# Performance work log

Measured on AMD Instinct MI355X. Metric: run time of the kernel, lower is better.

The kernel has to match this reference:

```python
import jax, jax.numpy as jnp
import numpy as np

N, IN, H, D, OUT = 2048, 256, 12, 32, 384
ALPHA = 0.2


def setup_inputs() -> dict:
    key = jax.random.key(0)
    ks = jax.random.split(key, 12)
    s = 0.05
    return {
        "x": jax.random.normal(ks[0], (N, IN), jnp.float32),
        "adj": jax.random.uniform(ks[1], (N, N), jnp.float32),  # all > 0 -> fully connected mask
        "W": jax.random.normal(ks[2], (H * D, IN), jnp.float32) * s,
        "attn_src": jax.random.normal(ks[3], (H, D), jnp.float32) * s,
        "attn_dst": jax.random.normal(ks[4], (H, D), jnp.float32) * s,
        "edge_W": jax.random.normal(ks[5], (H, 1), jnp.float32) * s,
        "edge_b": jax.random.normal(ks[6], (H,), jnp.float32) * s,
        "res_W": jax.random.normal(ks[7], (H * D, IN), jnp.float32) * s,
        "res_b": jax.random.normal(ks[8], (H * D,), jnp.float32) * s,
        "fus_W": jax.random.normal(ks[9], (OUT, H * D), jnp.float32) * s,
        "fus_b": jax.random.normal(ks[10], (OUT,), jnp.float32) * s,
    }


def reference(x, adj, W, attn_src, attn_dst, edge_W, edge_b, res_W, res_b, fus_W, fus_b):
    n = x.shape[0]
    h = (x @ W.T).reshape(n, H, D)                      # [N,H,D]
    a_src = jnp.einsum("nhd,hd->nh", h, attn_src)       # [N,H]
    a_dst = jnp.einsum("nhd,hd->nh", h, attn_dst)       # [N,H]
    attn = a_src[:, None, :] + a_dst[None, :, :]        # [N,N,H]
    # edge_encoder: Linear(1 -> H) applied to adj[...,None]
    attn = attn + adj[..., None] * edge_W.reshape(1, 1, H) + edge_b
    mask = (adj > 0)[..., None]                         # [N,N,1]
    attn = jnp.where(mask, attn, -jnp.inf)
    attn = jnp.where(attn >= 0, attn, ALPHA * attn)     # leaky_relu
    attn = jax.nn.softmax(attn, axis=1)                 # over source nodes j
    # dropout is identity in eval mode
    h_out = jnp.einsum("ijh,jhd->ihd", attn, h).reshape(n, H * D)
    h_out = h_out + x @ res_W.T + res_b                 # residual
    out = jax.nn.gelu(h_out @ fus_W.T + fus_b, approximate=False)
    return out
```

## Files before the change

### kernel.cpp

```cpp
#include <hip/hip_runtime.h>
#include <hip/hip_bf16.h>

#define NN 2048
#define NH 12
#define HD 32
#define CALL 384

typedef float f32x16 __attribute__((ext_vector_type(16)));
typedef _Float16 f16x4 __attribute__((ext_vector_type(4)));

static __device__ __forceinline__ f32x16 mfma8f16(f16x4 a, f16x4 b, f32x16 c) {
    return __builtin_amdgcn_mfma_f32_32x32x8f16(a, b, c, 0, 0, 0);
}
static __device__ __forceinline__ f16x4 u2f(uint2 u) {
    union { uint2 u2; f16x4 f; } c; c.u2 = u; return c.f;
}

__global__ __launch_bounds__(512) void gemm01(
    const float* __restrict__ A, const float* __restrict__ B0,
    const float* __restrict__ B1, const float* __restrict__ bias1,
    const float* __restrict__ attn_src, const float* __restrict__ attn_dst,
    _Float16* __restrict__ outT, float* __restrict__ outF,
    float* __restrict__ asrc, float* __restrict__ adstT)
{
    __shared__ __align__(16) char smem[17408];
    _Float16 (*As)[68] = (_Float16(*)[68])(smem);
    _Float16 (*Bs)[68] = (_Float16(*)[68])(smem + 8704);
    float* red = (float*)smem;

    const int t = threadIdx.x;
    const int w = t >> 6, l = t & 63, g = l >> 5, il = l & 31;
    const int q = w & 3, kg = w >> 2;
    const int m0 = blockIdx.x * 64, n0 = blockIdx.y * 64;
    const int mode = blockIdx.z;
    const float* B = mode ? B1 : B0;
    const int wr = (q >> 1) * 32, wc = (q & 1) * 32;
    const int ti = t >> 3, seg = t & 7;
    const int Kdim = 256;

    f32x16 acc;
#pragma unroll
    for (int r = 0; r < 16; ++r) acc[r] = 0.f;

#pragma unroll 1
    for (int ss = 0; ss < 4; ++ss) {
        const int kk = ss * 64;
        __syncthreads();
        {
            const float* Ap = A + (size_t)(m0 + ti) * Kdim + kk + seg * 8;
            float4 v0 = *reinterpret_cast<const float4*>(Ap);
            float4 v1 = *reinterpret_cast<const float4*>(Ap + 4);
            f16x4 lo = {(_Float16)v0.x, (_Float16)v0.y, (_Float16)v0.z, (_Float16)v0.w};
            f16x4 hi = {(_Float16)v1.x, (_Float16)v1.y, (_Float16)v1.z, (_Float16)v1.w};
            *reinterpret_cast<f16x4*>(&As[ti][seg * 8])     = lo;
            *reinterpret_cast<f16x4*>(&As[ti][seg * 8 + 4]) = hi;
        }
        {
            const float* Bp = B + (size_t)(n0 + ti) * Kdim + kk + seg * 8;
            float4 v0 = *reinterpret_cast<const float4*>(Bp);
            float4 v1 = *reinterpret_cast<const float4*>(Bp + 4);
            f16x4 lo = {(_Float16)v0.x, (_Float16)v0.y, (_Float16)v0.z, (_Float16)v0.w};
            f16x4 hi = {(_Float16)v1.x, (_Float16)v1.y, (_Float16)v1.z, (_Float16)v1.w};
            *reinterpret_cast<f16x4*>(&Bs[ti][seg * 8])     = lo;
            *reinterpret_cast<f16x4*>(&Bs[ti][seg * 8 + 4]) = hi;
        }
        __syncthreads();
#pragma unroll
        for (int kc = 0; kc < 4; ++kc) {
            f16x4 af = *reinterpret_cast<const f16x4*>(&As[wr + il][kg * 32 + kc * 8 + 4 * g]);
            f16x4 bf = *reinterpret_cast<const f16x4*>(&Bs[wc + il][kg * 32 + kc * 8 + 4 * g]);
            acc = mfma8f16(af, bf, acc);
        }
    }

    __syncthreads();
    if (kg == 1) {
#pragma unroll
        for (int r = 0; r < 16; ++r) red[(q * 16 + r) * 64 + l] = acc[r];
    }
    __syncthreads();
    if (kg != 0) return;
#pragma unroll
    for (int r = 0; r < 16; ++r) acc[r] += red[(q * 16 + r) * 64 + l];

    const int colg = n0 + wc + il;
    if (mode == 0) {
#pragma unroll
        for (int p = 0; p < 4; ++p) {
            const int row = m0 + wr + 8 * p + 4 * g;
            f16x4 v;
#pragma unroll
            for (int r = 0; r < 4; ++r) v[r] = (_Float16)acc[4 * p + r];
            *reinterpret_cast<f16x4*>(&outT[(size_t)colg * NN + row]) = v;
        }
        const int hstar = colg >> 5;
        const float sv = attn_src[hstar * HD + il];
        const float dv = attn_dst[hstar * HD + il];
        float ps[16], pd[16];
#pragma unroll
        for (int r = 0; r < 16; ++r) { ps[r] = acc[r] * sv; pd[r] = acc[r] * dv; }
#pragma unroll
        for (int m = 1; m <= 16; m <<= 1) {
#pragma unroll
            for (int r = 0; r < 16; ++r) {
                ps[r] += __shfl_xor(ps[r], m);
                pd[r] += __shfl_xor(pd[r], m);
            }
        }
        if (il == 0) {
#pragma unroll
            for (int r = 0; r < 16; ++r) {
                const int row = m0 + wr + (r & 3) + 8 * (r >> 2) + 4 * g;
                asrc[row * NH + hstar] = ps[r];
                adstT[(size_t)hstar * NN + row] = pd[r] * 1.44269504089f;
            }
        }
    } else {
        const float bs = bias1[colg];
#pragma unroll
        for (int r = 0; r < 16; ++r) {
            const int row = m0 + wr + (r & 3) + 8 * (r >> 2) + 4 * g;
            outF[(size_t)row * CALL + colg] = acc[r] + bs;
        }
    }
}

__global__ __launch_bounds__(512) void gemm2(
    const _Float16* __restrict__ A16, const float* __restrict__ B,
    const float* __restrict__ bias, float* __restrict__ outF)
{
    __shared__ __align__(16) char smem[17408];
    _Float16 (*As)[68] = (_Float16(*)[68])(smem);
    _Float16 (*Bs)[68] = (_Float16(*)[68])(smem + 8704);
    float* red = (float*)smem;

    const int t = threadIdx.x;
    const int w = t >> 6, l = t & 63, g = l >> 5, il = l & 31;
    const int q = w & 3, kg = w >> 2;
    const int m0 = blockIdx.x * 64, n0 = blockIdx.y * 64;
    const int wr = (q >> 1) * 32, wc = (q & 1) * 32;
    const int ti = t >> 3, seg = t & 7;
    const int Kdim = 384;

    f32x16 acc;
#pragma unroll
    for (int r = 0; r < 16; ++r) acc[r] = 0.f;

#pragma unroll 1
    for (int ss = 0; ss < 6; ++ss) {
        const int kk = ss * 64;
        __syncthreads();
        {
            const uint4 v = *reinterpret_cast<const uint4*>(A16 + (size_t)(m0 + ti) * Kdim + kk + seg * 8);
            *reinterpret_cast<uint2*>(&As[ti][seg * 8])     = make_uint2(v.x, v.y);
            *reinterpret_cast<uint2*>(&As[ti][seg * 8 + 4]) = make_uint2(v.z, v.w);
        }
        {
            const float* Bp = B + (size_t)(n0 + ti) * Kdim + kk + seg * 8;
            float4 v0 = *reinterpret_cast<const float4*>(Bp);
            float4 v1 = *reinterpret_cast<const float4*>(Bp + 4);
            f16x4 lo = {(_Float16)v0.x, (_Float16)v0.y, (_Float16)v0.z, (_Float16)v0.w};
            f16x4 hi = {(_Float16)v1.x, (_Float16)v1.y, (_Float16)v1.z, (_Float16)v1.w};
            *reinterpret_cast<f16x4*>(&Bs[ti][seg * 8])     = lo;
            *reinterpret_cast<f16x4*>(&Bs[ti][seg * 8 + 4]) = hi;
        }
        __syncthreads();
#pragma unroll
        for (int kc = 0; kc < 4; ++kc) {
            f16x4 af = *reinterpret_cast<const f16x4*>(&As[wr + il][kg * 32 + kc * 8 + 4 * g]);
            f16x4 bf = *reinterpret_cast<const f16x4*>(&Bs[wc + il][kg * 32 + kc * 8 + 4 * g]);
            acc = mfma8f16(af, bf, acc);
        }
    }

    __syncthreads();
    if (kg == 1) {
#pragma unroll
        for (int r = 0; r < 16; ++r) red[(q * 16 + r) * 64 + l] = acc[r];
    }
    __syncthreads();
    if (kg != 0) return;
#pragma unroll
    for (int r = 0; r < 16; ++r) acc[r] += red[(q * 16 + r) * 64 + l];

    const int colg = n0 + wc + il;
    const float bs = bias[colg];
#pragma unroll
    for (int r = 0; r < 16; ++r) {
        const int row = m0 + wr + (r & 3) + 8 * (r >> 2) + 4 * g;
        float vv = acc[r] + bs;
        vv = 0.5f * vv * (1.0f + erff(vv * 0.70710678118f));
        outF[(size_t)row * CALL + colg] = vv;
    }
}

__global__ __launch_bounds__(1024, 4) void attn6(
    const float* __restrict__ adj, const _Float16* __restrict__ hT,
    const float* __restrict__ asrc, const float* __restrict__ adstT,
    const float* __restrict__ eW, const float* __restrict__ eb,
    const float* __restrict__ res, _Float16* __restrict__ hsum)
{
    __shared__ __align__(16) char smem[55296];
    const int t = threadIdx.x;
    const int w = t >> 6, l = t & 63, g = l >> 5, il = l & 31;
    const int band = blockIdx.x & 63, hg = blockIdx.x >> 6;
    const int i0 = band * 32, h0 = hg * 3, c0 = hg * 96;

    float* adst_s = (float*)(smem + w * 1536);
    float* red    = (float*)smem;
    float* dsum_s = (float*)(smem + 49152);

    const float LOG2E = 1.44269504089f;
    float base_h[3], eWr[3];
#pragma unroll
    for (int hh = 0; hh < 3; ++hh) {
        base_h[hh] = (asrc[(size_t)(i0 + il) * NH + h0 + hh] + eb[h0 + hh]) * LOG2E;
        eWr[hh] = eW[h0 + hh] * LOG2E;
    }

    const int jbase = w * 128;
#pragma unroll
    for (int p = 0; p < 6; ++p) {
        const int idx = p * 64 + l;
        adst_s[idx] = adstT[(size_t)(h0 + (idx >> 7)) * NN + jbase + (idx & 127)];
    }

    f32x16 acc[3];
#pragma unroll
    for (int hh = 0; hh < 3; ++hh)
#pragma unroll
        for (int r = 0; r < 16; ++r) acc[hh][r] = 0.f;
    float dsum[3] = {0.f, 0.f, 0.f};

    const _Float16* hbase = hT  + (size_t)(c0 + il) * NN + jbase + 16 * g;
    const float*    abase = adj + (size_t)(i0 + il) * NN + jbase + 16 * g;

    float4 ajc[4], ajn[4];
#pragma unroll
    for (int p = 0; p < 4; ++p)
        ajc[p] = *reinterpret_cast<const float4*>(abase + 4 * p);

#pragma unroll 1
    for (int tl = 0; tl < 4; ++tl) {
        const int jo = tl * 32;
        if (tl < 3) {
#pragma unroll
            for (int p = 0; p < 4; ++p)
                ajn[p] = *reinterpret_cast<const float4*>(abase + jo + 32 + 4 * p);
        }
#pragma unroll
        for (int hh = 0; hh < 3; ++hh) {
            const _Float16* hp = hbase + (size_t)(hh * 32) * NN + jo;
            const uint4 hA = *reinterpret_cast<const uint4*>(hp);
            const uint4 hB = *reinterpret_cast<const uint4*>(hp + 8);
#pragma unroll
            for (int ks = 0; ks < 4; ++ks) {
                const float4 a4 = ajc[ks];
                const float4 ad = *reinterpret_cast<const float4*>(
                    &adst_s[hh * 128 + jo + 16 * g + 4 * ks]);
                f16x4 ef;
#pragma unroll
                for (int jj = 0; jj < 4; ++jj) {
                    const float ajv = (&a4.x)[jj];
                    float tt = fmaf(ajv, eWr[hh], base_h[hh] + (&ad.x)[jj]);
                    tt = fmaxf(tt, 0.2f * tt);
                    const float ee = ajv > 0.f ? exp2f(tt) : 0.f;
                    dsum[hh] += ee;
                    ef[jj] = (_Float16)ee;
                }
                const uint2 hu = (ks == 0) ? make_uint2(hA.x, hA.y)
                               : (ks == 1) ? make_uint2(hA.z, hA.w)
                               : (ks == 2) ? make_uint2(hB.x, hB.y)
                                           : make_uint2(hB.z, hB.w);
                acc[hh] = mfma8f16(ef, u2f(hu), acc[hh]);
            }
        }
#pragma unroll
        for (int p = 0; p < 4; ++p) ajc[p] = ajn[p];
    }

    __syncthreads();
#pragma unroll
    for (int hh = 0; hh < 3; ++hh) {
        const float dtot = dsum[hh] + __shfl_xor(dsum[hh], 32);
        if (g == 0) dsum_s[(w * 3 + hh) * 32 + il] = dtot;
    }
    if (w < 4) {
#pragma unroll
        for (int hh = 0; hh < 3; ++hh)
#pragma unroll
            for (int reg = 0; reg < 16; ++reg)
                red[((w * 3 + hh) * 16 + reg) * 64 + l] = acc[hh][reg];
    }
    __syncthreads();
    if (w >= 4 && w < 8) {
#pragma unroll
        for (int hh = 0; hh < 3; ++hh)
#pragma unroll
            for (int reg = 0; reg < 16; ++reg)
                red[(((w - 4) * 3 + hh) * 16 + reg) * 64 + l] += acc[hh][reg];
    }
    __syncthreads();
    if (w >= 8 && w < 12) {
#pragma unroll
        for (int hh = 0; hh < 3; ++hh)
#pragma unroll
            for (int reg = 0; reg < 16; ++reg)
                red[(((w - 8) * 3 + hh) * 16 + reg) * 64 + l] += acc[hh][reg];
    }
    __syncthreads();
    if (w >= 12) {
#pragma unroll
        for (int hh = 0; hh < 3; ++hh)
#pragma unroll
            for (int reg = 0; reg < 16; ++reg)
                red[(((w - 12) * 3 + hh) * 16 + reg) * 64 + l] += acc[hh][reg];
    }
    __syncthreads();

    {
        const int reg = w;
        const int row_off = (reg & 3) + 8 * (reg >> 2) + 4 * g;
        const int row = i0 + row_off;
#pragma unroll
        for (int hh = 0; hh < 3; ++hh) {
            float v = 0.f, d = 0.f;
#pragma unroll
            for (int p = 0; p < 4; ++p)
                v += red[((p * 3 + hh) * 16 + reg) * 64 + l];
#pragma unroll
            for (int ww = 0; ww < 16; ++ww)
                d += dsum_s[(ww * 3 + hh) * 32 + row_off];
            const int col = (h0 + hh) * 32 + il;
            hsum[(size_t)row * CALL + col] = (_Float16)(v / d + res[(size_t)row * CALL + col]);
        }
    }
}

extern "C" void kernel_launch(void* const* d_in, const int* in_sizes, int n_in,
                              void* d_out, int out_size, void* d_ws, size_t ws_size,
                              hipStream_t stream)
{
    const float* x        = (const float*)d_in[0];
    const float* adj      = (const float*)d_in[1];
    const float* W        = (const float*)d_in[2];
    const float* attn_src = (const float*)d_in[3];
    const float* attn_dst = (const float*)d_in[4];
    const float* edge_W   = (const float*)d_in[5];
    const float* edge_b   = (const float*)d_in[6];
    const float* res_W    = (const float*)d_in[7];
    const float* res_b    = (const float*)d_in[8];
    const float* fus_W    = (const float*)d_in[9];
    const float* fus_b    = (const float*)d_in[10];
    float* out = (float*)d_out;

    char* ws = (char*)d_ws;
    size_t off = 0;
    auto alloc = [&](size_t bytes) { void* p = ws + off; off = (off + bytes + 255) & ~(size_t)255; return p; };
    _Float16* hT    = (_Float16*)alloc((size_t)CALL * NN * 2);
    float*    res   = (float*)alloc((size_t)NN * CALL * 4);
    float*    asrc  = (float*)alloc((size_t)NN * NH * 4);
    float*    adstT = (float*)alloc((size_t)NH * NN * 4);
    _Float16* hsum  = (_Float16*)alloc((size_t)NN * CALL * 2);
    (void)ws_size;

    gemm01<<<dim3(32, 6, 2), dim3(512), 0, stream>>>(x, W, res_W, res_b, attn_src, attn_dst, hT, res, asrc, adstT);
    attn6<<<256, dim3(1024), 0, stream>>>(adj, hT, asrc, adstT, edge_W, edge_b, res, hsum);
    gemm2<<<dim3(32, 6), dim3(512), 0, stream>>>(hsum, fus_W, fus_b, out);
}
```

Baseline: 52.54 us.

## Split attention kernel to one head per block with 512-thread blocks

The attention kernel now assigns a single head per block across a 64x12 grid of 512-thread blocks, instead of three heads per block in 1024-thread blocks. Each wave covers 256 source nodes, and the adj loads are double-buffered across two 32-column tiles. The aim is more, smaller blocks with fewer accumulator registers and a shorter cross-wave reduction, for better occupancy and latency hiding. In exchange, the adjacency matrix is read once per head instead of once per three heads, which triples adj traffic. That traffic mostly hits L2 or the last-level cache.

After: 84.87 us. +61.6%, slower.

```diff
diff --git a/kernel.cpp b/kernel.cpp
--- a/kernel.cpp
+++ b/kernel.cpp
@@ -194,146 +194,126 @@
     }
 }
 
-__global__ __launch_bounds__(1024, 4) void attn6(
+__global__ __launch_bounds__(512, 6) void attn7(
     const float* __restrict__ adj, const _Float16* __restrict__ hT,
     const float* __restrict__ asrc, const float* __restrict__ adstT,
     const float* __restrict__ eW, const float* __restrict__ eb,
     const float* __restrict__ res, _Float16* __restrict__ hsum)
 {
-    __shared__ __align__(16) char smem[55296];
+    __shared__ __align__(16) char smem[17408];
     const int t = threadIdx.x;
     const int w = t >> 6, l = t & 63, g = l >> 5, il = l & 31;
-    const int band = blockIdx.x & 63, hg = blockIdx.x >> 6;
-    const int i0 = band * 32, h0 = hg * 3, c0 = hg * 96;
-
-    float* adst_s = (float*)(smem + w * 1536);
+    const int i0 = blockIdx.x * 32, h = blockIdx.y;
+    const int c0 = h * 32;
+
+    float* adst_s = (float*)(smem + w * 1024);
     float* red    = (float*)smem;
-    float* dsum_s = (float*)(smem + 49152);
+    float* dsum_s = (float*)(smem + 16384);
 
     const float LOG2E = 1.44269504089f;
-    float base_h[3], eWr[3];
-#pragma unroll
-    for (int hh = 0; hh < 3; ++hh) {
-        base_h[hh] = (asrc[(size_t)(i0 + il) * NH + h0 + hh] + eb[h0 + hh]) * LOG2E;
-        eWr[hh] = eW[h0 + hh] * LOG2E;
-    }
-
-    const int jbase = w * 128;
-#pragma unroll
-    for (int p = 0; p < 6; ++p) {
-        const int idx = p * 64 + l;
-        adst_s[idx] = adstT[(size_t)(h0 + (idx >> 7)) * NN + jbase + (idx & 127)];
-    }
-
-    f32x16 acc[3];
-#pragma unroll
-    for (int hh = 0; hh < 3; ++hh)
-#pragma unroll
-        for (int r = 0; r < 16; ++r) acc[hh][r] = 0.f;
-    float dsum[3] = {0.f, 0.f, 0.f};
+    const float base_h = (asrc[(size_t)(i0 + il) * NH + h] + eb[h]) * LOG2E;
+    const float eWr = eW[h] * LOG2E;
+
+    const int jbase = w * 256;
+#pragma unroll
+    for (int p = 0; p < 4; ++p)
+        adst_s[p * 64 + l] = adstT[(size_t)h * NN + jbase + p * 64 + l];
+
+    f32x16 acc;
+#pragma unroll
+    for (int r = 0; r < 16; ++r) acc[r] = 0.f;
+    float dsum = 0.f;
 
     const _Float16* hbase = hT  + (size_t)(c0 + il) * NN + jbase + 16 * g;
-    const float*    abase = adj + (size_t)(i0 + il) * NN + jbase + 16 * g;
-
-    float4 ajc[4], ajn[4];
-#pragma unroll
-    for (int p = 0; p < 4; ++p)
-        ajc[p] = *reinterpret_cast<const float4*>(abase + 4 * p);
+    const float*    arow  = adj + (size_t)(i0 + il) * NN + jbase + 16 * g;
+
+    float4 ajA[4], ajB[4];
+#pragma unroll
+    for (int p = 0; p < 4; ++p) ajA[p] = *reinterpret_cast<const float4*>(arow + 4 * p);
+#pragma unroll
+    for (int p = 0; p < 4; ++p) ajB[p] = *reinterpret_cast<const float4*>(arow + 32 + 4 * p);
+
+#define COMPUTE(JO, AJ)                                                              \
+    {                                                                                \
+        const int jo = (JO);                                                         \
+        const _Float16* hp = hbase + jo;                                             \
+        const uint4 hA = *reinterpret_cast<const uint4*>(hp);                        \
+        const uint4 hB = *reinterpret_cast<const uint4*>(hp + 8);                    \
+        _Pragma("unroll")                                                            \
+        for (int ks = 0; ks < 4; ++ks) {                                             \
+            const float4 a4 = AJ[ks];                                                \
+            const float4 ad = *reinterpret_cast<const float4*>(                      \
+                &adst_s[jo + 16 * g + 4 * ks]);                                      \
+            f16x4 ef;                                                                \
+            _Pragma("unroll")                                                        \
+            for (int jj = 0; jj < 4; ++jj) {                                         \
+                const float ajv = (&a4.x)[jj];                                       \
+                float tt = fmaf(ajv, eWr, base_h + (&ad.x)[jj]);                     \
+                tt = fmaxf(tt, 0.2f * tt);                                           \
+                const float ee = ajv > 0.f ? exp2f(tt) : 0.f;                        \
+                dsum += ee;                                                          \
+                ef[jj] = (_Float16)ee;                                               \
+            }                                                                        \
+            const uint2 hu = (ks == 0) ? make_uint2(hA.x, hA.y)                      \
+                           : (ks == 1) ? make_uint2(hA.z, hA.w)                      \
+                           : (ks == 2) ? make_uint2(hB.x, hB.y)                      \
+                                       : make_uint2(hB.z, hB.w);                     \
+            acc = mfma8f16(ef, u2f(hu), acc);                                        \
+        }                                                                            \
+    }
 
 #pragma unroll 1
-    for (int tl = 0; tl < 4; ++tl) {
-        const int jo = tl * 32;
-        if (tl < 3) {
+    for (int tp = 0; tp < 4; ++tp) {
+        const int jo0 = tp * 64;
+        COMPUTE(jo0, ajA);
+        if (tp < 3) {
 #pragma unroll
             for (int p = 0; p < 4; ++p)
-                ajn[p] = *reinterpret_cast<const float4*>(abase + jo + 32 + 4 * p);
-        }
-#pragma unroll
-        for (int hh = 0; hh < 3; ++hh) {
-            const _Float16* hp = hbase + (size_t)(hh * 32) * NN + jo;
-            const uint4 hA = *reinterpret_cast<const uint4*>(hp);
-            const uint4 hB = *reinterpret_cast<const uint4*>(hp + 8);
-#pragma unroll
-            for (int ks = 0; ks < 4; ++ks) {
-                const float4 a4 = ajc[ks];
-                const float4 ad = *reinterpret_cast<const float4*>(
-                    &adst_s[hh * 128 + jo + 16 * g + 4 * ks]);
-                f16x4 ef;
-#pragma unroll
-                for (int jj = 0; jj < 4; ++jj) {
-                    const float ajv = (&a4.x)[jj];
-                    float tt = fmaf(ajv, eWr[hh], base_h[hh] + (&ad.x)[jj]);
-                    tt = fmaxf(tt, 0.2f * tt);
-                    const float ee = ajv > 0.f ? exp2f(tt) : 0.f;
-                    dsum[hh] += ee;
-                    ef[jj] = (_Float16)ee;
-                }
-                const uint2 hu = (ks == 0) ? make_uint2(hA.x, hA.y)
-                               : (ks == 1) ? make_uint2(hA.z, hA.w)
-                               : (ks == 2) ? make_uint2(hB.x, hB.y)
-                                           : make_uint2(hB.z, hB.w);
-                acc[hh] = mfma8f16(ef, u2f(hu), acc[hh]);
-            }
-        }
-#pragma unroll
-        for (int p = 0; p < 4; ++p) ajc[p] = ajn[p];
-    }
-
-    __syncthreads();
-#pragma unroll
-    for (int hh = 0; hh < 3; ++hh) {
-        const float dtot = dsum[hh] + __shfl_xor(dsum[hh], 32);
-        if (g == 0) dsum_s[(w * 3 + hh) * 32 + il] = dtot;
+                ajA[p] = *reinterpret_cast<const float4*>(arow + jo0 + 64 + 4 * p);
+        }
+        COMPUTE(jo0 + 32, ajB);
+        if (tp < 3) {
+#pragma unroll
+            for (int p = 0; p < 4; ++p)
+                ajB[p] = *reinterpret_cast<const float4*>(arow + jo0 + 96 + 4 * p);
+        }
+    }
+#undef COMPUTE
+
+    __syncthreads();
+    {
+        const float dtot = dsum + __shfl_xor(dsum, 32);
+        if (g == 0) dsum_s[w * 32 + il] = dtot;
     }
     if (w < 4) {
 #pragma unroll
-        for (int hh = 0; hh < 3; ++hh)
-#pragma unroll
-            for (int reg = 0; reg < 16; ++reg)
-                red[((w * 3 + hh) * 16 + reg) * 64 + l] = acc[hh][reg];
-    }
-    __syncthreads();
-    if (w >= 4 && w < 8) {
-#pragma unroll
-        for (int hh = 0; hh < 3; ++hh)
-#pragma unroll
-            for (int reg = 0; reg < 16; ++reg)
-                red[(((w - 4) * 3 + hh) * 16 + reg) * 64 + l] += acc[hh][reg];
-    }
-    __syncthreads();
-    if (w >= 8 && w < 12) {
-#pragma unroll
-        for (int hh = 0; hh < 3; ++hh)
-#pragma unroll
-            for (int reg = 0; reg < 16; ++reg)
-                red[(((w - 8) * 3 + hh) * 16 + reg) * 64 + l] += acc[hh][reg];
-    }
-    __syncthreads();
-    if (w >= 12) {
-#pragma unroll
-        for (int hh = 0; hh < 3; ++hh)
-#pragma unroll
-            for (int reg = 0; reg < 16; ++reg)
-                red[(((w - 12) * 3 + hh) * 16 + reg) * 64 + l] += acc[hh][reg];
-    }
-    __syncthreads();
-
-    {
-        const int reg = w;
+        for (int r = 0; r < 16; ++r) red[(w * 16 + r) * 64 + l] = acc[r];
+    }
+    __syncthreads();
+    if (w >= 4) {
+#pragma unroll
+        for (int r = 0; r < 16; ++r) red[((w - 4) * 16 + r) * 64 + l] += acc[r];
+    }
+    __syncthreads();
+
+#pragma unroll
+    for (int rr = 0; rr < 2; ++rr) {
+        const int reg = w + rr * 8;
         const int row_off = (reg & 3) + 8 * (reg >> 2) + 4 * g;
         const int row = i0 + row_off;
-#pragma unroll
-        for (int hh = 0; hh < 3; ++hh) {
-            float v = 0.f, d = 0.f;
-#pragma unroll
-            for (int p = 0; p < 4; ++p)
-                v += red[((p * 3 + hh) * 16 + reg) * 64 + l];
-#pragma unroll
-            for (int ww = 0; ww < 16; ++ww)
-                d += dsum_s[(ww * 3 + hh) * 32 + row_off];
-            const int col = (h0 + hh) * 32 + il;
-            hsum[(size_t)row * CALL + col] = (_Float16)(v / d + res[(size_t)row * CALL + col]);
-        }
+        float v = 0.f, d = 0.f;
+#pragma unroll
+        for (int p = 0; p < 2; ++p)
+            v += red[((p + (reg >= 8 ? 0 : 0)) * 0 + ((reg & 7) < 4 ? 0 : 0)) ];
+        v = 0.f;
+#pragma unroll
+        for (int p = 0; p < 4; ++p)
+            v += red[(p * 16 + reg) * 64 + l];
+#pragma unroll
+        for (int ww = 0; ww < 8; ++ww)
+            d += dsum_s[ww * 32 + row_off];
+        const int col = c0 + il;
+        hsum[(size_t)row * CALL + col] = (_Float16)(v / d + res[(size_t)row * CALL + col]);
     }
 }
 
@@ -365,6 +345,6 @@
     (void)ws_size;
 
     gemm01<<<dim3(32, 6, 2), dim3(512), 0, stream>>>(x, W, res_W, res_b, attn_src, attn_dst, hT, res, asrc, adstT);
-    attn6<<<256, dim3(1024), 0, stream>>>(adj, hT, asrc, adstT, edge_W, edge_b, res, hsum);
+    attn7<<<dim3(64, NH), dim3(512), 0, stream>>>(adj, hT, asrc, adstT, edge_W, edge_b, res, hsum);
     gemm2<<<dim3(32, 6), dim3(512), 0, stream>>>(hsum, fus_W, fus_b, out);
 }
```

## Stream adj tiles into LDS via global_load_lds and use fast exp2/pkrtz conversion

Applied to the files above, without the earlier changes.

The attention kernel now prefetches each adj tile with direct global-to-LDS loads instead of holding the next tile in registers, then reads it back from LDS each iteration. It also switches to the hardware exp2 builtin, packs f16 values with cvt_pkrtz, and splits the denominator accumulation into four partial sums. The aim is to cut VGPR pressure and instruction count in the hot loop. In exchange, LDS use per block grows, which may limit occupancy, and waiting on vmcnt(0) at the top of each iteration serializes the prefetch.

Result: faster. 49.96 us (-4.9%).

```diff
diff --git a/kernel.cpp b/kernel.cpp
--- a/kernel.cpp
+++ b/kernel.cpp
@@ -8,12 +8,18 @@
 
 typedef float f32x16 __attribute__((ext_vector_type(16)));
 typedef _Float16 f16x4 __attribute__((ext_vector_type(4)));
+typedef __fp16 fp16x2 __attribute__((ext_vector_type(2)));
 
 static __device__ __forceinline__ f32x16 mfma8f16(f16x4 a, f16x4 b, f32x16 c) {
     return __builtin_amdgcn_mfma_f32_32x32x8f16(a, b, c, 0, 0, 0);
 }
 static __device__ __forceinline__ f16x4 u2f(uint2 u) {
     union { uint2 u2; f16x4 f; } c; c.u2 = u; return c.f;
+}
+static __device__ __forceinline__ void gload16(const float* gp, void* lp) {
+    __builtin_amdgcn_global_load_lds(
+        (const __attribute__((address_space(1))) unsigned int*)gp,
+        (__attribute__((address_space(3))) unsigned int*)lp, 16, 0, 0);
 }
 
 __global__ __launch_bounds__(512) void gemm01(
@@ -194,31 +200,38 @@
     }
 }
 
-__global__ __launch_bounds__(1024, 4) void attn6(
+__global__ __launch_bounds__(1024, 4) void attn13(
     const float* __restrict__ adj, const _Float16* __restrict__ hT,
     const float* __restrict__ asrc, const float* __restrict__ adstT,
     const float* __restrict__ eW, const float* __restrict__ eb,
     const float* __restrict__ res, _Float16* __restrict__ hsum)
 {
-    __shared__ __align__(16) char smem[55296];
+    __shared__ __align__(16) char smem[90112];
     const int t = threadIdx.x;
     const int w = t >> 6, l = t & 63, g = l >> 5, il = l & 31;
     const int band = blockIdx.x & 63, hg = blockIdx.x >> 6;
     const int i0 = band * 32, h0 = hg * 3, c0 = hg * 96;
 
-    float* adst_s = (float*)(smem + w * 1536);
+    char* slice   = smem + w * 5632;
+    char* adjb    = slice;
+    float* adst_s = (float*)(slice + 4096);
     float* red    = (float*)smem;
     float* dsum_s = (float*)(smem + 49152);
 
     const float LOG2E = 1.44269504089f;
+    const int jbase = w * 128;
+    const float* abase = adj + (size_t)(i0 + il) * NN + jbase + 16 * g;
+
+#pragma unroll
+    for (int p = 0; p < 4; ++p)
+        gload16(abase + 4 * p, adjb + p * 1024);
+
     float base_h[3], eWr[3];
 #pragma unroll
     for (int hh = 0; hh < 3; ++hh) {
         base_h[hh] = (asrc[(size_t)(i0 + il) * NH + h0 + hh] + eb[h0 + hh]) * LOG2E;
         eWr[hh] = eW[h0 + hh] * LOG2E;
     }
-
-    const int jbase = w * 128;
 #pragma unroll
     for (int p = 0; p < 6; ++p) {
         const int idx = p * 64 + l;
@@ -230,23 +243,25 @@
     for (int hh = 0; hh < 3; ++hh)
 #pragma unroll
         for (int r = 0; r < 16; ++r) acc[hh][r] = 0.f;
-    float dsum[3] = {0.f, 0.f, 0.f};
-
-    const _Float16* hbase = hT  + (size_t)(c0 + il) * NN + jbase + 16 * g;
-    const float*    abase = adj + (size_t)(i0 + il) * NN + jbase + 16 * g;
-
-    float4 ajc[4], ajn[4];
-#pragma unroll
-    for (int p = 0; p < 4; ++p)
-        ajc[p] = *reinterpret_cast<const float4*>(abase + 4 * p);
+    float4 dsumv[3];
+#pragma unroll
+    for (int hh = 0; hh < 3; ++hh) dsumv[hh] = make_float4(0.f, 0.f, 0.f, 0.f);
+
+    const _Float16* hbase = hT + (size_t)(c0 + il) * NN + jbase + 16 * g;
 
 #pragma unroll 1
     for (int tl = 0; tl < 4; ++tl) {
         const int jo = tl * 32;
+        asm volatile("s_waitcnt vmcnt(0)" ::: "memory");
+        const float4 aj0 = *reinterpret_cast<const float4*>(adjb + 0 * 1024 + l * 16);
+        const float4 aj1 = *reinterpret_cast<const float4*>(adjb + 1 * 1024 + l * 16);
+        const float4 aj2 = *reinterpret_cast<const float4*>(adjb + 2 * 1024 + l * 16);
+        const float4 aj3 = *reinterpret_cast<const float4*>(adjb + 3 * 1024 + l * 16);
+        asm volatile("s_waitcnt lgkmcnt(0)" ::: "memory");
         if (tl < 3) {
 #pragma unroll
             for (int p = 0; p < 4; ++p)
-                ajn[p] = *reinterpret_cast<const float4*>(abase + jo + 32 + 4 * p);
+                gload16(abase + jo + 32 + 4 * p, adjb + p * 1024);
         }
 #pragma unroll
         for (int hh = 0; hh < 3; ++hh) {
@@ -255,34 +270,36 @@
             const uint4 hB = *reinterpret_cast<const uint4*>(hp + 8);
 #pragma unroll
             for (int ks = 0; ks < 4; ++ks) {
-                const float4 a4 = ajc[ks];
+                const float4 a4 = (ks == 0) ? aj0 : (ks == 1) ? aj1 : (ks == 2) ? aj2 : aj3;
                 const float4 ad = *reinterpret_cast<const float4*>(
                     &adst_s[hh * 128 + jo + 16 * g + 4 * ks]);
-                f16x4 ef;
+                float e0, e1, e2, e3;
 #pragma unroll
                 for (int jj = 0; jj < 4; ++jj) {
                     const float ajv = (&a4.x)[jj];
                     float tt = fmaf(ajv, eWr[hh], base_h[hh] + (&ad.x)[jj]);
                     tt = fmaxf(tt, 0.2f * tt);
-                    const float ee = ajv > 0.f ? exp2f(tt) : 0.f;
-                    dsum[hh] += ee;
-                    ef[jj] = (_Float16)ee;
+                    const float ee = ajv > 0.f ? __builtin_amdgcn_exp2f(tt) : 0.f;
+                    (&dsumv[hh].x)[jj] += ee;
+                    (jj == 0 ? e0 : jj == 1 ? e1 : jj == 2 ? e2 : e3) = ee;
                 }
+                union { fp16x2 h2[2]; f16x4 h4; } u;
+                u.h2[0] = __builtin_amdgcn_cvt_pkrtz(e0, e1);
+                u.h2[1] = __builtin_amdgcn_cvt_pkrtz(e2, e3);
                 const uint2 hu = (ks == 0) ? make_uint2(hA.x, hA.y)
                                : (ks == 1) ? make_uint2(hA.z, hA.w)
                                : (ks == 2) ? make_uint2(hB.x, hB.y)
                                            : make_uint2(hB.z, hB.w);
-                acc[hh] = mfma8f16(ef, u2f(hu), acc[hh]);
+                acc[hh] = mfma8f16(u.h4, u2f(hu), acc[hh]);
             }
         }
-#pragma unroll
-        for (int p = 0; p < 4; ++p) ajc[p] = ajn[p];
     }
 
     __syncthreads();
 #pragma unroll
     for (int hh = 0; hh < 3; ++hh) {
-        const float dtot = dsum[hh] + __shfl_xor(dsum[hh], 32);
+        const float ds = (dsumv[hh].x + dsumv[hh].y) + (dsumv[hh].z + dsumv[hh].w);
+        const float dtot = ds + __shfl_xor(ds, 32);
         if (g == 0) dsum_s[(w * 3 + hh) * 32 + il] = dtot;
     }
     if (w < 4) {
@@ -365,6 +382,6 @@
     (void)ws_size;
 
     gemm01<<<dim3(32, 6, 2), dim3(512), 0, stream>>>(x, W, res_W, res_b, attn_src, attn_dst, hT, res, asrc, adstT);
-    attn6<<<256, dim3(1024), 0, stream>>>(adj, hT, asrc, adstT, edge_W, edge_b, res, hsum);
+    attn13<<<256, dim3(1024), 0, stream>>>(adj, hT, asrc, adstT, edge_W, edge_b, res, hsum);
     gemm2<<<dim3(32, 6), dim3(512), 0, stream>>>(hsum, fus_W, fus_b, out);
 }
```
